# Kernel optimization log

Hardware: AMD Instinct MI355X
Metric: run time of the kernel (lower is better)

## Reference

```python
import jax, jax.numpy as jnp
import numpy as np

B, T, NB, H = 1024, 128, 13, 128
T_IN = 64  # input_timesteps


def setup_inputs() -> dict:
    key = jax.random.key(0)
    ks = jax.random.split(key, 7)
    s = 1.0 / np.sqrt(H)
    return {
        "x": jax.random.normal(ks[0], (B, T, NB), dtype=jnp.float32),
        "W_ih": jax.random.normal(ks[1], (4 * H, NB), dtype=jnp.float32) * s,
        "W_hh": jax.random.normal(ks[2], (4 * H, H), dtype=jnp.float32) * s,
        "b_ih": jax.random.normal(ks[3], (4 * H,), dtype=jnp.float32) * s,
        "b_hh": jax.random.normal(ks[4], (4 * H,), dtype=jnp.float32) * s,
        "W_out": jax.random.normal(ks[5], (NB, H), dtype=jnp.float32) * s,
        "b_out": jax.random.normal(ks[6], (NB,), dtype=jnp.float32) * s,
    }


def _lstm_cell(x_t, h, c, W_ih, W_hh, b_ih, b_hh):
    # PyTorch nn.LSTM gate order: input, forget, cell(g), output
    gates = x_t @ W_ih.T + h @ W_hh.T + (b_ih + b_hh)  # [B, 4H]
    i, f, g, o = jnp.split(gates, 4, axis=-1)
    i = jax.nn.sigmoid(i)
    f = jax.nn.sigmoid(f)
    g = jnp.tanh(g)
    o = jax.nn.sigmoid(o)
    c_new = f * c + i * g
    h_new = o * jnp.tanh(c_new)
    return h_new, c_new


def reference(x, W_ih, W_hh, b_ih, b_hh, W_out, b_out):
    # forward_train with teacher_forcing=False, gp_enabled=False:
    # 1) teacher-fed LSTM over x[:, :T_IN]
    batch = x.shape[0]
    h0 = jnp.zeros((batch, H), dtype=x.dtype)
    c0 = jnp.zeros((batch, H), dtype=x.dtype)

    def step_teacher(carry, x_t):
        h, c = carry
        h, c = _lstm_cell(x_t, h, c, W_ih, W_hh, b_ih, b_hh)
        y = h @ W_out.T + b_out  # [B, NB]
        return (h, c), y

    (h, c), ys1 = jax.lax.scan(step_teacher, (h0, c0),
                               jnp.swapaxes(x[:, :T_IN], 0, 1))  # ys1: [T_IN, B, NB]

    remaining = T - T_IN - 1

    def step_auto(carry, _):
        h, c, inp = carry
        h, c = _lstm_cell(inp, h, c, W_ih, W_hh, b_ih, b_hh)
        y = h @ W_out.T + b_out
        return (h, c, y), y

    _, ys2 = jax.lax.scan(step_auto, (h, c, x[:, T_IN]), None, length=remaining)

    out = jnp.concatenate([
        x[:, 0:1],
        jnp.swapaxes(ys1, 0, 1),
        jnp.swapaxes(ys2, 0, 1),
    ], axis=1)  # [B, T, NB]
    return out
```

## Files before the change

kernel.cpp:

```cpp
#include <hip/hip_runtime.h>
#include <math.h>

#define BATCH 1024
#define TT    128
#define NBI   13
#define HH    128
#define T_INP 64
#define BB    4
#define NBLK  (BATCH/BB)

#define LOG2E 1.4426950408889634f
#define C2L   2.8853900817779268f
#define C4L   5.7707801635558537f

typedef _Float16 half8 __attribute__((ext_vector_type(8)));
typedef float    f32x4 __attribute__((ext_vector_type(4)));

__device__ __forceinline__ unsigned short f16b(float v) {
    return __builtin_bit_cast(unsigned short, (_Float16)v);
}
__device__ __forceinline__ float rcpf_(float x) { return __builtin_amdgcn_rcpf(x); }

#if __has_builtin(__builtin_amdgcn_exp2f)
__device__ __forceinline__ float exp2_(float x) { return __builtin_amdgcn_exp2f(x); }
#else
__device__ __forceinline__ float exp2_(float x) { return __expf(x * 0.6931471805599453f); }
#endif

__device__ __forceinline__ void barrier_lds() {
    asm volatile("s_waitcnt lgkmcnt(0)" ::: "memory");
    __builtin_amdgcn_sched_barrier(0);
    __builtin_amdgcn_s_barrier();
    __builtin_amdgcn_sched_barrier(0);
}

#define WS_WHH   0
#define WS_WHAT  131072
#define WS_WIHP  262144
#define WS_WOUT  294912
#define WS_BT    299008
#define WS_BA    301056

__global__ void fold_kernel(const float* __restrict__ W_ih,
                            const float* __restrict__ W_hh,
                            const float* __restrict__ b_ih,
                            const float* __restrict__ b_hh,
                            const float* __restrict__ W_out,
                            const float* __restrict__ b_out,
                            unsigned char* __restrict__ ws)
{
    const int j = blockIdx.x;
    const int k = threadIdx.x;
    unsigned short* whh16  = (unsigned short*)(ws + WS_WHH);
    unsigned short* what16 = (unsigned short*)(ws + WS_WHAT);
    unsigned short* wihp16 = (unsigned short*)(ws + WS_WIHP);
    unsigned short* wout16 = (unsigned short*)(ws + WS_WOUT);
    float* bias_t = (float*)(ws + WS_BT);
    float* bias_a = (float*)(ws + WS_BA);

    const int gate = j >> 7;
    const float sc = (gate == 2) ? (2.0f * LOG2E) : (-LOG2E);

    float whh = W_hh[j * HH + k];
    float acc = whh;
#pragma unroll
    for (int m = 0; m < NBI; ++m)
        acc += W_ih[j * NBI + m] * W_out[m * HH + k];
    whh16[j * HH + k]  = f16b(sc * whh);
    what16[j * HH + k] = f16b(sc * acc);

    if (k < 32) wihp16[j * 32 + k] = (k < NBI) ? f16b(sc * W_ih[j * NBI + k]) : (unsigned short)0;
    if (k == 0) {
        float bt = b_ih[j] + b_hh[j];
        bias_t[j] = sc * bt;
        float ba = bt;
#pragma unroll
        for (int m = 0; m < NBI; ++m) ba += W_ih[j * NBI + m] * b_out[m];
        bias_a[j] = sc * ba;
    }
    if (j < 16) wout16[j * HH + k] = (j < NBI) ? f16b(W_out[j * HH + k]) : (unsigned short)0;
}

#define MFMA16(A, B, C) __builtin_amdgcn_mfma_f32_16x16x32_f16((A), (B), (C), 0, 0, 0)

__global__ __launch_bounds__(512, 2)
void lstm_main(const float* __restrict__ x,
               const float* __restrict__ b_out,
               const unsigned char* __restrict__ ws,
               float* __restrict__ out)
{
    const int j  = threadIdx.x;
    const int w  = j >> 6;
    const int l  = j & 63;
    const int q  = l >> 4;
    const int cb = l & 15;
    const int bbase = blockIdx.x * BB;

    const unsigned short* whh16  = (const unsigned short*)(ws + WS_WHH);
    const unsigned short* what16 = (const unsigned short*)(ws + WS_WHAT);
    const unsigned short* wihp16 = (const unsigned short*)(ws + WS_WIHP);
    const unsigned short* wout16 = (const unsigned short*)(ws + WS_WOUT);
    const float* btfp = (const float*)(ws + WS_BT);
    const float* bafp = (const float*)(ws + WS_BA);

    __shared__ half8 h_s[2][16][17];
    __shared__ half8 x_s[2][4][17];
    __shared__ float g_sf[4 * 520];

    const int cbn = (cb < BB) ? cb : 16;

    half8 wf[4][4];
    half8 wxf[4];
    half8 wof[4];
    f32x4 binit[4];
#pragma unroll
    for (int a = 0; a < 4; ++a) {
        const int row = 64 * w + 16 * a + cb;
#pragma unroll
        for (int kk = 0; kk < 4; ++kk)
            wf[a][kk] = *(const half8*)(whh16 + row * HH + 32 * kk + 8 * q);
        wxf[a] = *(const half8*)(wihp16 + row * 32 + 8 * q);
#pragma unroll
        for (int r = 0; r < 4; ++r)
            binit[a][r] = btfp[64 * w + 16 * a + 4 * q + r];
    }
    const bool projw = (w == 7);
#pragma unroll
    for (int kk = 0; kk < 4; ++kk)
        wof[kk] = *(const half8*)(wout16 + cb * HH + 32 * kk + 8 * q);

    f32x4 bo4;
#pragma unroll
    for (int r = 0; r < 4; ++r) {
        const int m = 4 * q + r;
        bo4[r] = (m < NBI) ? b_out[m] : 0.0f;
    }
    const f32x4 z4 = {0.f, 0.f, 0.f, 0.f};
    float* pob = out + (size_t)(bbase + (cb & 3)) * TT * NBI;

    const int uu = j & 127;
    const int ub = j >> 7;
    const float* gme = g_sf + ub * 520 + uu;

    const int  sid = j - 384;
    const bool stg = (sid >= 0) && (sid < BB * NBI);
    int s_b = 0, s_m = 0;
    const float* xp0 = x;
    float xa_h = 0.f;
    if (stg) { s_b = sid / 13; s_m = sid - 13 * s_b;
               xp0 = x + (size_t)(bbase + s_b) * TT * NBI + s_m; }

    {
        half8* hz = (half8*)h_s;
        hz[j] = (half8)(_Float16)0.0f;
        if (j < 32) hz[512 + j] = (half8)(_Float16)0.0f;
        half8* xz = (half8*)x_s;
        if (j < 136) xz[j] = (half8)(_Float16)0.0f;
    }
    __syncthreads();
    if (stg) {
        float v = xp0[0];
        ((_Float16*)&x_s[0][s_m >> 3][s_b])[s_m & 7] = (_Float16)v;
        out[(size_t)(bbase + s_b) * TT * NBI + s_m] = v;
        xa_h = xp0[NBI];
    }
    __syncthreads();

    float c = 0.0f;
    int cur = 0;

    for (int t = 0; t <= T_INP; ++t) {
        const int nxt = cur ^ 1;

        float xa_p = 0.f;
        if (stg && t + 2 <= T_INP) xa_p = xp0[(t + 2) * NBI];

        half8 xf  = x_s[cur][q][cbn];
        half8 hb0 = h_s[cur][q][cbn];
        half8 hb1 = h_s[cur][4 + q][cbn];
        half8 hb2 = h_s[cur][8 + q][cbn];
        half8 hb3 = h_s[cur][12 + q][cbn];

        f32x4 a0 = MFMA16(wxf[0], xf, binit[0]);
        f32x4 a1 = MFMA16(wxf[1], xf, binit[1]);
        f32x4 a2 = MFMA16(wxf[2], xf, binit[2]);
        f32x4 a3 = MFMA16(wxf[3], xf, binit[3]);
        a0 = MFMA16(wf[0][0], hb0, a0); a1 = MFMA16(wf[1][0], hb0, a1);
        a2 = MFMA16(wf[2][0], hb0, a2); a3 = MFMA16(wf[3][0], hb0, a3);
        a0 = MFMA16(wf[0][1], hb1, a0); a1 = MFMA16(wf[1][1], hb1, a1);
        a2 = MFMA16(wf[2][1], hb1, a2); a3 = MFMA16(wf[3][1], hb1, a3);
        a0 = MFMA16(wf[0][2], hb2, a0); a1 = MFMA16(wf[1][2], hb2, a1);
        a2 = MFMA16(wf[2][2], hb2, a2); a3 = MFMA16(wf[3][2], hb2, a3);
        a0 = MFMA16(wf[0][3], hb3, a0); a1 = MFMA16(wf[1][3], hb3, a1);
        a2 = MFMA16(wf[2][3], hb3, a2); a3 = MFMA16(wf[3][3], hb3, a3);

        f32x4 pacc = z4;
        if (projw) {
            pacc = MFMA16(wof[0], hb0, z4);
            pacc = MFMA16(wof[1], hb1, pacc);
            pacc = MFMA16(wof[2], hb2, pacc);
            pacc = MFMA16(wof[3], hb3, pacc);
        }

        if (cb < BB) {
            float* gb = g_sf + cb * 520 + 64 * w + 4 * q;
            *(f32x4*)(gb)      = a0;
            *(f32x4*)(gb + 16) = a1;
            *(f32x4*)(gb + 32) = a2;
            *(f32x4*)(gb + 48) = a3;
        }
        if (projw && t >= 1 && cb < BB) {
#pragma unroll
            for (int r = 0; r < 4; ++r) {
                const int m = 4 * q + r;
                if (m < NBI) pob[t * NBI + m] = pacc[r] + bo4[r];
            }
        }
        barrier_lds();

        {
            float gi = gme[0], gf = gme[128], gg = gme[256], go = gme[384];
            float ig = rcpf_(1.0f + exp2_(gi));
            float fg = rcpf_(1.0f + exp2_(gf));
            float rg = rcpf_(exp2_(gg) + 1.0f);
            float gp = C2L - C4L * rg;
            float og = rcpf_(1.0f + exp2_(go));
            float cn = fg * c + ig * gp;
            c = cn;
            float ec = exp2_(cn);
            float hv = og * (1.0f - 2.0f * rcpf_(ec + 1.0f));
            ((_Float16*)&h_s[nxt][uu >> 3][ub])[uu & 7] = (_Float16)hv;
        }
        if (stg && t + 1 <= T_INP) {
            ((_Float16*)&x_s[nxt][s_m >> 3][s_b])[s_m & 7] = (_Float16)xa_h;
            xa_h = xa_p;
        }
        barrier_lds();
        cur = nxt;
    }

#pragma unroll
    for (int a = 0; a < 4; ++a) {
        const int row = 64 * w + 16 * a + cb;
#pragma unroll
        for (int kk = 0; kk < 4; ++kk)
            wf[a][kk] = *(const half8*)(what16 + row * HH + 32 * kk + 8 * q);
#pragma unroll
        for (int r = 0; r < 4; ++r)
            binit[a][r] = bafp[64 * w + 16 * a + 4 * q + r];
    }

    for (int t = T_INP + 1; t < TT - 1; ++t) {
        const int nxt = cur ^ 1;

        half8 hb0 = h_s[cur][q][cbn];
        half8 hb1 = h_s[cur][4 + q][cbn];
        half8 hb2 = h_s[cur][8 + q][cbn];
        half8 hb3 = h_s[cur][12 + q][cbn];

        f32x4 a0 = MFMA16(wf[0][0], hb0, binit[0]);
        f32x4 a1 = MFMA16(wf[1][0], hb0, binit[1]);
        f32x4 a2 = MFMA16(wf[2][0], hb0, binit[2]);
        f32x4 a3 = MFMA16(wf[3][0], hb0, binit[3]);
        a0 = MFMA16(wf[0][1], hb1, a0); a1 = MFMA16(wf[1][1], hb1, a1);
        a2 = MFMA16(wf[2][1], hb1, a2); a3 = MFMA16(wf[3][1], hb1, a3);
        a0 = MFMA16(wf[0][2], hb2, a0); a1 = MFMA16(wf[1][2], hb2, a1);
        a2 = MFMA16(wf[2][2], hb2, a2); a3 = MFMA16(wf[3][2], hb2, a3);
        a0 = MFMA16(wf[0][3], hb3, a0); a1 = MFMA16(wf[1][3], hb3, a1);
        a2 = MFMA16(wf[2][3], hb3, a2); a3 = MFMA16(wf[3][3], hb3, a3);

        f32x4 pacc = z4;
        if (projw) {
            pacc = MFMA16(wof[0], hb0, z4);
            pacc = MFMA16(wof[1], hb1, pacc);
            pacc = MFMA16(wof[2], hb2, pacc);
            pacc = MFMA16(wof[3], hb3, pacc);
        }

        if (cb < BB) {
            float* gb = g_sf + cb * 520 + 64 * w + 4 * q;
            *(f32x4*)(gb)      = a0;
            *(f32x4*)(gb + 16) = a1;
            *(f32x4*)(gb + 32) = a2;
            *(f32x4*)(gb + 48) = a3;
        }
        if (projw && cb < BB) {
#pragma unroll
            for (int r = 0; r < 4; ++r) {
                const int m = 4 * q + r;
                if (m < NBI) pob[t * NBI + m] = pacc[r] + bo4[r];
            }
        }
        barrier_lds();

        {
            float gi = gme[0], gf = gme[128], gg = gme[256], go = gme[384];
            float ig = rcpf_(1.0f + exp2_(gi));
            float fg = rcpf_(1.0f + exp2_(gf));
            float rg = rcpf_(exp2_(gg) + 1.0f);
            float gp = C2L - C4L * rg;
            float og = rcpf_(1.0f + exp2_(go));
            float cn = fg * c + ig * gp;
            c = cn;
            float ec = exp2_(cn);
            float hv = og * (1.0f - 2.0f * rcpf_(ec + 1.0f));
            ((_Float16*)&h_s[nxt][uu >> 3][ub])[uu & 7] = (_Float16)hv;
        }
        barrier_lds();
        cur = nxt;
    }

    if (projw) {
        half8 hb0 = h_s[cur][q][cbn];
        half8 hb1 = h_s[cur][4 + q][cbn];
        half8 hb2 = h_s[cur][8 + q][cbn];
        half8 hb3 = h_s[cur][12 + q][cbn];
        f32x4 pacc = MFMA16(wof[0], hb0, z4);
        pacc = MFMA16(wof[1], hb1, pacc);
        pacc = MFMA16(wof[2], hb2, pacc);
        pacc = MFMA16(wof[3], hb3, pacc);
        if (cb < BB) {
#pragma unroll
            for (int r = 0; r < 4; ++r) {
                const int m = 4 * q + r;
                if (m < NBI) pob[(TT - 1) * NBI + m] = pacc[r] + bo4[r];
            }
        }
    }
}

extern "C" void kernel_launch(void* const* d_in, const int* in_sizes, int n_in,
                              void* d_out, int out_size, void* d_ws, size_t ws_size,
                              hipStream_t stream)
{
    const float* x     = (const float*)d_in[0];
    const float* W_ih  = (const float*)d_in[1];
    const float* W_hh  = (const float*)d_in[2];
    const float* b_ih  = (const float*)d_in[3];
    const float* b_hh  = (const float*)d_in[4];
    const float* W_out = (const float*)d_in[5];
    const float* b_out = (const float*)d_in[6];
    float* out = (float*)d_out;
    unsigned char* ws = (unsigned char*)d_ws;

    fold_kernel<<<512, HH, 0, stream>>>(W_ih, W_hh, b_ih, b_hh, W_out, b_out, ws);
    lstm_main<<<NBLK, 512, 0, stream>>>(x, b_out, ws, out);
}
```

Baseline: 174.4 us.

## Split gate rows across 16 waves with 1024-thread blocks

Doubles the threads per block from 512 to 1024, so each wave computes 32 gate rows (two MFMA chains) instead of 64 (four chains). This shortens the serial MFMA chain per wave on each recurrent step and spreads the weight registers across more waves. In exchange, half the threads sit idle during the elementwise cell update, and barriers now synchronise 16 waves instead of 8. Launch bounds of (1024, 2) also tighten the register budget and may limit occupancy.

```diff
diff --git a/kernel.cpp b/kernel.cpp
--- a/kernel.cpp
+++ b/kernel.cpp
@@ -8,6 +8,7 @@
 #define T_INP 64
 #define BB    4
 #define NBLK  (BATCH/BB)
+#define NTHR  1024
 
 #define LOG2E 1.4426950408889634f
 #define C2L   2.8853900817779268f
@@ -83,7 +84,7 @@
 
 #define MFMA16(A, B, C) __builtin_amdgcn_mfma_f32_16x16x32_f16((A), (B), (C), 0, 0, 0)
 
-__global__ __launch_bounds__(512, 2)
+__global__ __launch_bounds__(NTHR, 2)
 void lstm_main(const float* __restrict__ x,
                const float* __restrict__ b_out,
                const unsigned char* __restrict__ ws,
@@ -109,22 +110,22 @@
 
     const int cbn = (cb < BB) ? cb : 16;
 
-    half8 wf[4][4];
-    half8 wxf[4];
+    half8 wf[2][4];
+    half8 wxf[2];
     half8 wof[4];
-    f32x4 binit[4];
-#pragma unroll
-    for (int a = 0; a < 4; ++a) {
-        const int row = 64 * w + 16 * a + cb;
+    f32x4 binit[2];
+#pragma unroll
+    for (int a = 0; a < 2; ++a) {
+        const int row = 32 * w + 16 * a + cb;
 #pragma unroll
         for (int kk = 0; kk < 4; ++kk)
             wf[a][kk] = *(const half8*)(whh16 + row * HH + 32 * kk + 8 * q);
         wxf[a] = *(const half8*)(wihp16 + row * 32 + 8 * q);
 #pragma unroll
         for (int r = 0; r < 4; ++r)
-            binit[a][r] = btfp[64 * w + 16 * a + 4 * q + r];
-    }
-    const bool projw = (w == 7);
+            binit[a][r] = btfp[32 * w + 16 * a + 4 * q + r];
+    }
+    const bool projw = (w == 14);
 #pragma unroll
     for (int kk = 0; kk < 4; ++kk)
         wof[kk] = *(const half8*)(wout16 + cb * HH + 32 * kk + 8 * q);
@@ -138,11 +139,12 @@
     const f32x4 z4 = {0.f, 0.f, 0.f, 0.f};
     float* pob = out + (size_t)(bbase + (cb & 3)) * TT * NBI;
 
+    const bool doU = (j < 512);
     const int uu = j & 127;
-    const int ub = j >> 7;
+    const int ub = (j >> 7) & 3;
     const float* gme = g_sf + ub * 520 + uu;
 
-    const int  sid = j - 384;
+    const int  sid = j - 960;
     const bool stg = (sid >= 0) && (sid < BB * NBI);
     int s_b = 0, s_m = 0;
     const float* xp0 = x;
@@ -152,8 +154,7 @@
 
     {
         half8* hz = (half8*)h_s;
-        hz[j] = (half8)(_Float16)0.0f;
-        if (j < 32) hz[512 + j] = (half8)(_Float16)0.0f;
+        if (j < 544) hz[j] = (half8)(_Float16)0.0f;
         half8* xz = (half8*)x_s;
         if (j < 136) xz[j] = (half8)(_Float16)0.0f;
     }
@@ -183,16 +184,10 @@
 
         f32x4 a0 = MFMA16(wxf[0], xf, binit[0]);
         f32x4 a1 = MFMA16(wxf[1], xf, binit[1]);
-        f32x4 a2 = MFMA16(wxf[2], xf, binit[2]);
-        f32x4 a3 = MFMA16(wxf[3], xf, binit[3]);
         a0 = MFMA16(wf[0][0], hb0, a0); a1 = MFMA16(wf[1][0], hb0, a1);
-        a2 = MFMA16(wf[2][0], hb0, a2); a3 = MFMA16(wf[3][0], hb0, a3);
         a0 = MFMA16(wf[0][1], hb1, a0); a1 = MFMA16(wf[1][1], hb1, a1);
-        a2 = MFMA16(wf[2][1], hb1, a2); a3 = MFMA16(wf[3][1], hb1, a3);
         a0 = MFMA16(wf[0][2], hb2, a0); a1 = MFMA16(wf[1][2], hb2, a1);
-        a2 = MFMA16(wf[2][2], hb2, a2); a3 = MFMA16(wf[3][2], hb2, a3);
         a0 = MFMA16(wf[0][3], hb3, a0); a1 = MFMA16(wf[1][3], hb3, a1);
-        a2 = MFMA16(wf[2][3], hb3, a2); a3 = MFMA16(wf[3][3], hb3, a3);
 
         f32x4 pacc = z4;
         if (projw) {
@@ -203,11 +198,9 @@
         }
 
         if (cb < BB) {
-            float* gb = g_sf + cb * 520 + 64 * w + 4 * q;
+            float* gb = g_sf + cb * 520 + 32 * w + 4 * q;
             *(f32x4*)(gb)      = a0;
             *(f32x4*)(gb + 16) = a1;
-            *(f32x4*)(gb + 32) = a2;
-            *(f32x4*)(gb + 48) = a3;
         }
         if (projw && t >= 1 && cb < BB) {
 #pragma unroll
@@ -218,7 +211,7 @@
         }
         barrier_lds();
 
-        {
+        if (doU) {
             float gi = gme[0], gf = gme[128], gg = gme[256], go = gme[384];
             float ig = rcpf_(1.0f + exp2_(gi));
             float fg = rcpf_(1.0f + exp2_(gf));
@@ -240,14 +233,14 @@
     }
 
 #pragma unroll
-    for (int a = 0; a < 4; ++a) {
-        const int row = 64 * w + 16 * a + cb;
+    for (int a = 0; a < 2; ++a) {
+        const int row = 32 * w + 16 * a + cb;
 #pragma unroll
         for (int kk = 0; kk < 4; ++kk)
             wf[a][kk] = *(const half8*)(what16 + row * HH + 32 * kk + 8 * q);
 #pragma unroll
         for (int r = 0; r < 4; ++r)
-            binit[a][r] = bafp[64 * w + 16 * a + 4 * q + r];
+            binit[a][r] = bafp[32 * w + 16 * a + 4 * q + r];
     }
 
     for (int t = T_INP + 1; t < TT - 1; ++t) {
@@ -260,14 +253,9 @@
 
         f32x4 a0 = MFMA16(wf[0][0], hb0, binit[0]);
         f32x4 a1 = MFMA16(wf[1][0], hb0, binit[1]);
-        f32x4 a2 = MFMA16(wf[2][0], hb0, binit[2]);
-        f32x4 a3 = MFMA16(wf[3][0], hb0, binit[3]);
         a0 = MFMA16(wf[0][1], hb1, a0); a1 = MFMA16(wf[1][1], hb1, a1);
-        a2 = MFMA16(wf[2][1], hb1, a2); a3 = MFMA16(wf[3][1], hb1, a3);
         a0 = MFMA16(wf[0][2], hb2, a0); a1 = MFMA16(wf[1][2], hb2, a1);
-        a2 = MFMA16(wf[2][2], hb2, a2); a3 = MFMA16(wf[3][2], hb2, a3);
         a0 = MFMA16(wf[0][3], hb3, a0); a1 = MFMA16(wf[1][3], hb3, a1);
-        a2 = MFMA16(wf[2][3], hb3, a2); a3 = MFMA16(wf[3][3], hb3, a3);
 
         f32x4 pacc = z4;
         if (projw) {
@@ -278,11 +266,9 @@
         }
 
         if (cb < BB) {
-            float* gb = g_sf + cb * 520 + 64 * w + 4 * q;
+            float* gb = g_sf + cb * 520 + 32 * w + 4 * q;
             *(f32x4*)(gb)      = a0;
             *(f32x4*)(gb + 16) = a1;
-            *(f32x4*)(gb + 32) = a2;
-            *(f32x4*)(gb + 48) = a3;
         }
         if (projw && cb < BB) {
 #pragma unroll
@@ -293,7 +279,7 @@
         }
         barrier_lds();
 
-        {
+        if (doU) {
             float gi = gme[0], gf = gme[128], gg = gme[256], go = gme[384];
             float ig = rcpf_(1.0f + exp2_(gi));
             float fg = rcpf_(1.0f + exp2_(gf));
@@ -344,5 +330,5 @@
     unsigned char* ws = (unsigned char*)d_ws;
 
     fold_kernel<<<512, HH, 0, stream>>>(W_ih, W_hh, b_ih, b_hh, W_out, b_out, ws);
-    lstm_main<<<NBLK, 512, 0, stream>>>(x, b_out, ws, out);
-}
+    lstm_main<<<NBLK, NTHR, 0, stream>>>(x, b_out, ws, out);
+}
```

Result: slower. 184.1 us (+5.5%).
